# Kernel tuning notes

Measured on AMD Instinct MI355X. Metric: run time of the kernel, lower is better.

Reference implementation:

```python
import jax, jax.numpy as jnp
import numpy as np

B, N_IN, N_UP, SEQ, CIN, COUT = 8, 7056, 28224, 9, 64, 32
E = 3 * N_UP  # nnz of sparse upsample matrix


def setup_inputs() -> dict:
    key = jax.random.key(0)
    ks = jax.random.split(key, 7)
    x = jax.random.normal(ks[0], (B, N_IN, CIN), dtype=jnp.float32)
    val = jax.random.uniform(ks[1], (E,), dtype=jnp.float32)
    # xavier-uniform-ish init for Linear(SEQ*CIN -> COUT)
    lim = float(np.sqrt(6.0 / (SEQ * CIN + COUT)))
    W = jax.random.uniform(ks[2], (SEQ * CIN, COUT), minval=-lim, maxval=lim, dtype=jnp.float32)
    b = jnp.zeros((COUT,), dtype=jnp.float32)
    row = jax.random.randint(ks[3], (E,), 0, N_UP)
    col = jax.random.randint(ks[4], (E,), 0, N_IN)
    indices = jax.random.randint(ks[5], (N_UP, SEQ), 0, N_UP)
    return {"x": x, "val": val, "W": W, "b": b, "row": row, "col": col, "indices": indices}


def reference(x, val, W, b, row, col, indices):
    # Pool: out[b, row, :] += x[b, col, :] * val   (sparse upsample, dim_size = N_UP)
    gathered = x[:, col, :] * val[None, :, None]              # [B, E, CIN]
    pooled = jnp.zeros((x.shape[0], N_UP, x.shape[2]), dtype=x.dtype)
    pooled = pooled.at[:, row, :].add(gathered)               # [B, N_UP, CIN]
    # SpiralConv: spiral neighborhood gather then Linear + ReLU
    spiral = pooled[:, indices.reshape(-1), :]                # [B, N_UP*SEQ, CIN]
    spiral = spiral.reshape(x.shape[0], N_UP, SEQ * x.shape[2])  # [B, N_UP, SEQ*CIN]
    out = jnp.einsum('bnf,fo->bno', spiral, W) + b            # [B, N_UP, COUT]
    return jax.nn.relu(out)
```

## Files before the change

kernel.cpp:

```cpp
#include <hip/hip_runtime.h>
#include <hip/hip_bf16.h>

namespace {
constexpr int kB    = 8;
constexpr int kNIn  = 7056;
constexpr int kNUp  = 28224;
constexpr int kSeq  = 9;
constexpr int kCin  = 64;
constexpr int kCout = 32;
constexpr int kE    = 3 * kNUp;
constexpr int kMRows = kB * kNUp;
constexpr int kTilesPerB = kNUp / 16;
constexpr int kWFragN = 18 * 2 * 64 * 8;
constexpr int kCap   = 24;

constexpr size_t kOffPool   = 0;
constexpr size_t kOffWfrag  = 28901376;
constexpr size_t kOffCur    = kOffWfrag + 36864;
constexpr size_t kOffBucket = kOffCur + 112896;
}

typedef __attribute__((ext_vector_type(8))) short short8;
typedef __attribute__((ext_vector_type(4))) float f32x4;

__device__ __forceinline__ unsigned short f32_to_bf16(float f) {
    unsigned int u = __float_as_uint(f);
    u += 0x7fffu + ((u >> 16) & 1u);
    return (unsigned short)(u >> 16);
}

__global__ __launch_bounds__(256) void zero_kernel(int* __restrict__ cursor) {
    int i = blockIdx.x * 256 + threadIdx.x;
    if (i < kNUp) cursor[i] = 0;
}

__global__ __launch_bounds__(256) void prep_kernel(const float* __restrict__ W,
                                                   unsigned short* __restrict__ wfrag,
                                                   const int* __restrict__ row,
                                                   const int* __restrict__ col,
                                                   const float* __restrict__ val,
                                                   int* __restrict__ cursor,
                                                   uint2* __restrict__ bucket) {
    int bid = blockIdx.x;
    if (bid < kWFragN / 256) {
        int i  = bid * 256 + threadIdx.x;
        int j  = i & 7;
        int l  = (i >> 3) & 63;
        int ct = (i >> 9) & 1;
        int ks = i >> 10;
        int k  = ks * 32 + (l >> 4) * 8 + j;
        int o  = ct * 16 + (l & 15);
        wfrag[i] = f32_to_bf16(W[k * kCout + o]);
    } else {
        int e = (bid - kWFragN / 256) * 256 + threadIdx.x;
        if (e >= kE) return;
        int r = row[e];
        int slot = atomicAdd(&cursor[r], 1);
        if ((unsigned)slot < (unsigned)kCap)
            bucket[(size_t)r * kCap + slot] = make_uint2((unsigned)col[e], __float_as_uint(val[e]));
    }
}

__global__ __launch_bounds__(256) void pool_gather(const float* __restrict__ x,
                                                   const int* __restrict__ cursor,
                                                   const uint2* __restrict__ bucket,
                                                   unsigned short* __restrict__ poolb) {
    int t  = threadIdx.x;
    int c4 = t & 15;
    int b  = blockIdx.x & 7;
    int rb = blockIdx.x >> 3;
    int r  = rb * 16 + (t >> 4);
    int n  = min(cursor[r], kCap);
    const uint2* bk = bucket + (size_t)r * kCap;
    const float* xb = x + (size_t)b * kNIn * kCin + (size_t)c4 * 4;

    f32x4 acc = {0.f, 0.f, 0.f, 0.f};
#pragma unroll
    for (int p = 0; p < 4; ++p) {
        if (2 * p < n) {
            uint4 q = *reinterpret_cast<const uint4*>(bk + 2 * p);
            unsigned c0 = min(q.x, (unsigned)(kNIn - 1));
            float    v0 = __uint_as_float(q.y);
            unsigned c1 = min(q.z, (unsigned)(kNIn - 1));
            float    v1 = (2 * p + 1 < n) ? __uint_as_float(q.w) : 0.f;
            f32x4 xv0 = *reinterpret_cast<const f32x4*>(xb + (size_t)c0 * kCin);
            f32x4 xv1 = *reinterpret_cast<const f32x4*>(xb + (size_t)c1 * kCin);
#pragma unroll
            for (int j = 0; j < 4; ++j)
                acc[j] = fmaf(xv1[j], v1, fmaf(xv0[j], v0, acc[j]));
        }
    }
    for (int k = 8; k < n; ++k) {
        uint2 ev = bk[k];
        float v = __uint_as_float(ev.y);
        f32x4 xv = *reinterpret_cast<const f32x4*>(xb + (size_t)ev.x * kCin);
#pragma unroll
        for (int j = 0; j < 4; ++j) acc[j] = fmaf(xv[j], v, acc[j]);
    }
    ushort4 o;
    o.x = f32_to_bf16(acc[0]);
    o.y = f32_to_bf16(acc[1]);
    o.z = f32_to_bf16(acc[2]);
    o.w = f32_to_bf16(acc[3]);
    *reinterpret_cast<ushort4*>(poolb + ((size_t)b * kNUp + r) * kCin + c4 * 4) = o;
}

__global__ __launch_bounds__(256) void gemm_mfma(const unsigned short* __restrict__ poolb,
                                                 const unsigned short* __restrict__ wfrag,
                                                 const float* __restrict__ bias,
                                                 const int* __restrict__ indices,
                                                 float* __restrict__ out) {
    __shared__ short8 Bs[10 * 2 * 64];
    int t = threadIdx.x;
    const short8* wf = (const short8*)wfrag;

    int l = t & 63;
    int w = t >> 6;
    int m  = l & 15;
    int kg = l >> 4;
    int bid = blockIdx.x;
    int wk = (bid & 7) * (gridDim.x >> 3) + (bid >> 3);
    int mtile = wk * 4 + w;
    int b  = mtile / kTilesPerB;
    int nn = (mtile - b * kTilesPerB) * 16 + m;
    const unsigned short* pb = poolb + (size_t)b * kNUp * kCin;

    int idxs[kSeq];
#pragma unroll
    for (int s = 0; s < kSeq; ++s) idxs[s] = indices[nn * kSeq + s];

    short8 A0[kSeq], A1[kSeq];
#pragma unroll
    for (int s = 0; s < kSeq; ++s) {
        const short8* ar = (const short8*)(pb + (size_t)idxs[s] * kCin);
        A0[s] = ar[kg];
        A1[s] = ar[4 + kg];
    }
    __builtin_amdgcn_sched_barrier(0);

#pragma unroll
    for (int i = 0; i < 5; ++i) Bs[i * 256 + t] = wf[i * 256 + t];

    float bs0 = bias[m];
    float bs1 = bias[16 + m];
    f32x4 acc0 = {0.f, 0.f, 0.f, 0.f};
    f32x4 acc1 = {0.f, 0.f, 0.f, 0.f};

    __syncthreads();

#pragma unroll
    for (int s = 0; s < 5; ++s) {
        short8 b00 = Bs[(4 * s + 0) * 64 + l];
        short8 b01 = Bs[(4 * s + 1) * 64 + l];
        short8 b10 = Bs[(4 * s + 2) * 64 + l];
        short8 b11 = Bs[(4 * s + 3) * 64 + l];
        acc0 = __builtin_amdgcn_mfma_f32_16x16x32_bf16(A0[s], b00, acc0, 0, 0, 0);
        acc1 = __builtin_amdgcn_mfma_f32_16x16x32_bf16(A0[s], b01, acc1, 0, 0, 0);
        acc0 = __builtin_amdgcn_mfma_f32_16x16x32_bf16(A1[s], b10, acc0, 0, 0, 0);
        acc1 = __builtin_amdgcn_mfma_f32_16x16x32_bf16(A1[s], b11, acc1, 0, 0, 0);
    }

    __syncthreads();
#pragma unroll
    for (int i = 0; i < 4; ++i) Bs[i * 256 + t] = wf[1280 + i * 256 + t];
    __syncthreads();

#pragma unroll
    for (int s = 5; s < kSeq; ++s) {
        short8 b00 = Bs[(4 * (s - 5) + 0) * 64 + l];
        short8 b01 = Bs[(4 * (s - 5) + 1) * 64 + l];
        short8 b10 = Bs[(4 * (s - 5) + 2) * 64 + l];
        short8 b11 = Bs[(4 * (s - 5) + 3) * 64 + l];
        acc0 = __builtin_amdgcn_mfma_f32_16x16x32_bf16(A0[s], b00, acc0, 0, 0, 0);
        acc1 = __builtin_amdgcn_mfma_f32_16x16x32_bf16(A0[s], b01, acc1, 0, 0, 0);
        acc0 = __builtin_amdgcn_mfma_f32_16x16x32_bf16(A1[s], b10, acc0, 0, 0, 0);
        acc1 = __builtin_amdgcn_mfma_f32_16x16x32_bf16(A1[s], b11, acc1, 0, 0, 0);
    }

    int orow0 = mtile * 16 + kg * 4;
#pragma unroll
    for (int r = 0; r < 4; ++r) {
        size_t orow = (size_t)(orow0 + r) * kCout;
        out[orow + m]      = fmaxf(acc0[r] + bs0, 0.f);
        out[orow + 16 + m] = fmaxf(acc1[r] + bs1, 0.f);
    }
}

extern "C" void kernel_launch(void* const* d_in, const int* in_sizes, int n_in,
                              void* d_out, int out_size, void* d_ws, size_t ws_size,
                              hipStream_t stream) {
    const float* x    = (const float*)d_in[0];
    const float* val  = (const float*)d_in[1];
    const float* W    = (const float*)d_in[2];
    const float* bias = (const float*)d_in[3];
    const int* row     = (const int*)d_in[4];
    const int* col     = (const int*)d_in[5];
    const int* indices = (const int*)d_in[6];
    float* out = (float*)d_out;

    char* wsb = (char*)d_ws;
    unsigned short* poolb = (unsigned short*)(wsb + kOffPool);
    unsigned short* wfrag = (unsigned short*)(wsb + kOffWfrag);
    int* cursor  = (int*)(wsb + kOffCur);
    uint2* bucket = (uint2*)(wsb + kOffBucket);

    zero_kernel<<<(kNUp + 255) / 256, 256, 0, stream>>>(cursor);

    constexpr int prep_blocks = kWFragN / 256 + (kE + 255) / 256;
    prep_kernel<<<prep_blocks, 256, 0, stream>>>(W, wfrag, row, col, val, cursor, bucket);

    pool_gather<<<kNUp / 16 * kB, 256, 0, stream>>>(x, cursor, bucket, poolb);

    gemm_mfma<<<(kMRows / 16) / 4, 256, 0, stream>>>(poolb, wfrag, bias, indices, out);
}
```

Measured before the change: 78.19 us.

## Interleave batch in pooled layout and share spiral gathers across batches via LDS

Result: no change. 77.55 us (-0.8%).

```diff
diff --git a/kernel.cpp b/kernel.cpp
--- a/kernel.cpp
+++ b/kernel.cpp
@@ -6,11 +6,10 @@
 constexpr int kNIn  = 7056;
 constexpr int kNUp  = 28224;
 constexpr int kSeq  = 9;
+constexpr int kCout = 32;
 constexpr int kCin  = 64;
-constexpr int kCout = 32;
 constexpr int kE    = 3 * kNUp;
-constexpr int kMRows = kB * kNUp;
-constexpr int kTilesPerB = kNUp / 16;
+constexpr int kNTiles = kNUp / 16;
 constexpr int kWFragN = 18 * 2 * 64 * 8;
 constexpr int kCap   = 24;
 
@@ -102,7 +101,7 @@
     o.y = f32_to_bf16(acc[1]);
     o.z = f32_to_bf16(acc[2]);
     o.w = f32_to_bf16(acc[3]);
-    *reinterpret_cast<ushort4*>(poolb + ((size_t)b * kNUp + r) * kCin + c4 * 4) = o;
+    *reinterpret_cast<ushort4*>(poolb + ((size_t)r * 8 + b) * 64 + c4 * 4) = o;
 }
 
 __global__ __launch_bounds__(256) void gemm_mfma(const unsigned short* __restrict__ poolb,
@@ -111,78 +110,102 @@
                                                  const int* __restrict__ indices,
                                                  float* __restrict__ out) {
     __shared__ short8 Bs[10 * 2 * 64];
+    __shared__ short8 As[2][16 * 64];
     int t = threadIdx.x;
+    int l = t & 63, w = t >> 6, m = l & 15, kg = l >> 4;
+    int ntile = blockIdx.x;
     const short8* wf = (const short8*)wfrag;
 
-    int l = t & 63;
-    int w = t >> 6;
-    int m  = l & 15;
-    int kg = l >> 4;
-    int bid = blockIdx.x;
-    int wk = (bid & 7) * (gridDim.x >> 3) + (bid >> 3);
-    int mtile = wk * 4 + w;
-    int b  = mtile / kTilesPerB;
-    int nn = (mtile - b * kTilesPerB) * 16 + m;
-    const unsigned short* pb = poolb + (size_t)b * kNUp * kCin;
-
     int idxs[kSeq];
 #pragma unroll
-    for (int s = 0; s < kSeq; ++s) idxs[s] = indices[nn * kSeq + s];
-
-    short8 A0[kSeq], A1[kSeq];
+    for (int s = 0; s < kSeq; ++s) idxs[s] = indices[(ntile * 16 + m) * kSeq + s];
+
+    int b0 = 2 * w, b1 = 2 * w + 1;
+    float bsv0 = bias[m];
+    float bsv1 = bias[16 + m];
+
+    {
+        short8 pf[4];
+#pragma unroll
+        for (int i = 0; i < 4; ++i) {
+            int rm = 4 * w + i;
+            int rowid = __shfl(idxs[0], rm);
+            pf[i] = *(const short8*)(poolb + (size_t)rowid * 512 + l * 8);
+        }
+#pragma unroll
+        for (int i = 0; i < 4; ++i) {
+            int rm = 4 * w + i;
+            As[0][rm * 64 + (l ^ (rm & 7))] = pf[i];
+        }
+    }
+#pragma unroll
+    for (int i = 0; i < 5; ++i) Bs[i * 256 + t] = wf[i * 256 + t];
+    __syncthreads();
+
+    f32x4 accA0 = {0.f, 0.f, 0.f, 0.f}, accA1 = {0.f, 0.f, 0.f, 0.f};
+    f32x4 accB0 = {0.f, 0.f, 0.f, 0.f}, accB1 = {0.f, 0.f, 0.f, 0.f};
+
 #pragma unroll
     for (int s = 0; s < kSeq; ++s) {
-        const short8* ar = (const short8*)(pb + (size_t)idxs[s] * kCin);
-        A0[s] = ar[kg];
-        A1[s] = ar[4 + kg];
-    }
-    __builtin_amdgcn_sched_barrier(0);
-
-#pragma unroll
-    for (int i = 0; i < 5; ++i) Bs[i * 256 + t] = wf[i * 256 + t];
-
-    float bs0 = bias[m];
-    float bs1 = bias[16 + m];
-    f32x4 acc0 = {0.f, 0.f, 0.f, 0.f};
-    f32x4 acc1 = {0.f, 0.f, 0.f, 0.f};
-
-    __syncthreads();
-
-#pragma unroll
-    for (int s = 0; s < 5; ++s) {
-        short8 b00 = Bs[(4 * s + 0) * 64 + l];
-        short8 b01 = Bs[(4 * s + 1) * 64 + l];
-        short8 b10 = Bs[(4 * s + 2) * 64 + l];
-        short8 b11 = Bs[(4 * s + 3) * 64 + l];
-        acc0 = __builtin_amdgcn_mfma_f32_16x16x32_bf16(A0[s], b00, acc0, 0, 0, 0);
-        acc1 = __builtin_amdgcn_mfma_f32_16x16x32_bf16(A0[s], b01, acc1, 0, 0, 0);
-        acc0 = __builtin_amdgcn_mfma_f32_16x16x32_bf16(A1[s], b10, acc0, 0, 0, 0);
-        acc1 = __builtin_amdgcn_mfma_f32_16x16x32_bf16(A1[s], b11, acc1, 0, 0, 0);
-    }
-
-    __syncthreads();
-#pragma unroll
-    for (int i = 0; i < 4; ++i) Bs[i * 256 + t] = wf[1280 + i * 256 + t];
-    __syncthreads();
-
-#pragma unroll
-    for (int s = 5; s < kSeq; ++s) {
-        short8 b00 = Bs[(4 * (s - 5) + 0) * 64 + l];
-        short8 b01 = Bs[(4 * (s - 5) + 1) * 64 + l];
-        short8 b10 = Bs[(4 * (s - 5) + 2) * 64 + l];
-        short8 b11 = Bs[(4 * (s - 5) + 3) * 64 + l];
-        acc0 = __builtin_amdgcn_mfma_f32_16x16x32_bf16(A0[s], b00, acc0, 0, 0, 0);
-        acc1 = __builtin_amdgcn_mfma_f32_16x16x32_bf16(A0[s], b01, acc1, 0, 0, 0);
-        acc0 = __builtin_amdgcn_mfma_f32_16x16x32_bf16(A1[s], b10, acc0, 0, 0, 0);
-        acc1 = __builtin_amdgcn_mfma_f32_16x16x32_bf16(A1[s], b11, acc1, 0, 0, 0);
-    }
-
-    int orow0 = mtile * 16 + kg * 4;
-#pragma unroll
-    for (int r = 0; r < 4; ++r) {
-        size_t orow = (size_t)(orow0 + r) * kCout;
-        out[orow + m]      = fmaxf(acc0[r] + bs0, 0.f);
-        out[orow + 16 + m] = fmaxf(acc1[r] + bs1, 0.f);
+        if (s == 5) {
+#pragma unroll
+            for (int i = 0; i < 4; ++i) Bs[i * 256 + t] = wf[1280 + i * 256 + t];
+            __syncthreads();
+        }
+        short8 pf[4];
+        if (s < kSeq - 1) {
+#pragma unroll
+            for (int i = 0; i < 4; ++i) {
+                int rm = 4 * w + i;
+                int rowid = __shfl(idxs[s + 1], rm);
+                pf[i] = *(const short8*)(poolb + (size_t)rowid * 512 + l * 8);
+            }
+        }
+
+        int sl = (s < 5) ? s : (s - 5);
+        short8 w00 = Bs[(4 * sl + 0) * 64 + l];
+        short8 w01 = Bs[(4 * sl + 1) * 64 + l];
+        short8 w10 = Bs[(4 * sl + 2) * 64 + l];
+        short8 w11 = Bs[(4 * sl + 3) * 64 + l];
+
+        const short8* Ab = &As[s & 1][0];
+        int mswz = m & 7;
+        short8 a0 = Ab[m * 64 + ((b0 * 8 + kg) ^ mswz)];
+        short8 a1 = Ab[m * 64 + ((b0 * 8 + 4 + kg) ^ mswz)];
+        short8 c0 = Ab[m * 64 + ((b1 * 8 + kg) ^ mswz)];
+        short8 c1 = Ab[m * 64 + ((b1 * 8 + 4 + kg) ^ mswz)];
+
+        accA0 = __builtin_amdgcn_mfma_f32_16x16x32_bf16(a0, w00, accA0, 0, 0, 0);
+        accA1 = __builtin_amdgcn_mfma_f32_16x16x32_bf16(a0, w01, accA1, 0, 0, 0);
+        accA0 = __builtin_amdgcn_mfma_f32_16x16x32_bf16(a1, w10, accA0, 0, 0, 0);
+        accA1 = __builtin_amdgcn_mfma_f32_16x16x32_bf16(a1, w11, accA1, 0, 0, 0);
+        accB0 = __builtin_amdgcn_mfma_f32_16x16x32_bf16(c0, w00, accB0, 0, 0, 0);
+        accB1 = __builtin_amdgcn_mfma_f32_16x16x32_bf16(c0, w01, accB1, 0, 0, 0);
+        accB0 = __builtin_amdgcn_mfma_f32_16x16x32_bf16(c1, w10, accB0, 0, 0, 0);
+        accB1 = __builtin_amdgcn_mfma_f32_16x16x32_bf16(c1, w11, accB1, 0, 0, 0);
+
+        if (s < kSeq - 1) {
+#pragma unroll
+            for (int i = 0; i < 4; ++i) {
+                int rm = 4 * w + i;
+                As[(s + 1) & 1][rm * 64 + (l ^ (rm & 7))] = pf[i];
+            }
+        }
+        __syncthreads();
+    }
+
+#pragma unroll
+    for (int bb = 0; bb < 2; ++bb) {
+        int b = (bb == 0) ? b0 : b1;
+        f32x4 v0 = (bb == 0) ? accA0 : accB0;
+        f32x4 v1 = (bb == 0) ? accA1 : accB1;
+        int R0 = b * kNUp + ntile * 16 + kg * 4;
+#pragma unroll
+        for (int r4 = 0; r4 < 4; ++r4) {
+            size_t orow = (size_t)(R0 + r4) * kCout;
+            out[orow + m]      = fmaxf(v0[r4] + bsv0, 0.f);
+            out[orow + 16 + m] = fmaxf(v1[r4] + bsv1, 0.f);
+        }
     }
 }
 
@@ -211,5 +234,5 @@
 
     pool_gather<<<kNUp / 16 * kB, 256, 0, stream>>>(x, cursor, bucket, poolb);
 
-    gemm_mfma<<<(kMRows / 16) / 4, 256, 0, stream>>>(poolb, wfrag, bias, indices, out);
-}
+    gemm_mfma<<<kNTiles, 256, 0, stream>>>(poolb, wfrag, bias, indices, out);
+}
```
